# Performance work log

Hardware: AMD Instinct MI355X
Metric: run time of the kernel (lower is better)

## Reference

```python
import jax, jax.numpy as jnp
import numpy as np

N_LAB = 8   # number of distinct node labels
E_LAB = 3   # number of distinct edge labels (bond types 1..3; 0 = no edge)
N_NODES = 95
SINKHORN_ITERS = 10


def _symmetric_adj(key, n, max_lab):
    a = jax.random.randint(key, (n, n), 0, max_lab + 1).astype(jnp.int32)
    a = jnp.triu(a, 1)
    return a + a.T  # symmetric, zero diagonal


def setup_inputs() -> dict:
    key = jax.random.key(0)
    k1, k2, k3, k4, k5, k6 = jax.random.split(key, 6)
    A1 = _symmetric_adj(k1, N_NODES, E_LAB)
    A2 = _symmetric_adj(k2, N_NODES, E_LAB)
    l1 = jax.random.randint(k3, (N_NODES,), 0, N_LAB).astype(jnp.int32)
    l2 = jax.random.randint(k4, (N_NODES,), 0, N_LAB).astype(jnp.int32)
    n_pair = N_LAB * (N_LAB - 1) // 2
    e_pair = E_LAB * (E_LAB - 1) // 2
    node_weighs = (0.011 * jax.random.uniform(k5, (n_pair + 1,))).at[-1].set(0.03)
    edge_weighs = (0.011 * jax.random.uniform(k6, (e_pair + 1,))).at[-1].set(0.02)
    return {"A1": A1, "A2": A2, "l1": l1, "l2": l2,
            "node_weighs": node_weighs.astype(jnp.float32),
            "edge_weighs": edge_weighs.astype(jnp.float32)}


def _from_weighs_to_costs(node_weighs, edge_weighs):
    cn = jax.nn.relu(node_weighs)
    ce = jax.nn.relu(edge_weighs)
    iu_n = jnp.triu_indices(N_LAB, 1)
    node_costs = jnp.zeros((N_LAB, N_LAB), cn.dtype).at[iu_n].set(cn[:-1])
    node_costs = node_costs + node_costs.T
    iu_e = jnp.triu_indices(E_LAB, 1)
    edge_costs = jnp.zeros((E_LAB, E_LAB), ce.dtype).at[iu_e].set(ce[:-1])
    edge_costs = edge_costs + edge_costs.T
    return node_costs, cn[-1], edge_costs, ce[-1]


def _eps_assign2(M, n_iter):
    # Sinkhorn-style alternating row/column normalization
    for _ in range(n_iter):
        M = M / M.sum(axis=1, keepdims=True)
        M = M / M.sum(axis=0, keepdims=True)
    return M


def _ged_forward(A1, A2, l1, l2, node_weighs, edge_weighs):
    node_costs, nodeInsDel, edge_costs, edgeInsDel = _from_weighs_to_costs(node_weighs, edge_weighs)
    n = A1.shape[0]
    m = A2.shape[0]
    Np, Mp = n + 1, m + 1

    # Padded adjacency (extra epsilon row/col, label 0 = no edge)
    a1 = jnp.zeros((Np, Np), jnp.int32).at[:n, :n].set(A1)
    a2 = jnp.zeros((Mp, Mp), jnp.int32).at[:m, :m].set(A2)

    # Full edge-pair cost table over labels {0..E}: 0<->lab = ins/del, lab<->lab' = subst
    EC = jnp.zeros((E_LAB + 1, E_LAB + 1), node_costs.dtype)
    EC = EC.at[1:, 1:].set(edge_costs)
    EC = EC.at[0, 1:].set(edgeInsDel).at[1:, 0].set(edgeInsDel)
    # (original: edgeInsDel * XOR(nonzero) + sum_{k!=l} edge_costs[k,l] * 1[a1==k+1] 1[a2==l+1])

    # T[i,j,k,l] = EC[a1[i,j], a2[k,l]]; flatten as C[j*Mp+k, i*Mp+l]
    T = EC[a1[:, :, None, None], a2[None, None, :, :]]          # (Np,Np,Mp,Mp)
    Cbig = jnp.transpose(T, (1, 2, 0, 3)).reshape(Np * Mp, Np * Mp)

    # Node cost vector on the diagonal (LSAPE layout)
    NCx = jnp.zeros((N_LAB + 1, N_LAB + 1), node_costs.dtype)
    NCx = NCx.at[:N_LAB, :N_LAB].set(node_costs)
    NCx = NCx.at[N_LAB, :N_LAB].set(nodeInsDel).at[:N_LAB, N_LAB].set(nodeInsDel)
    l1e = jnp.concatenate([l1, jnp.array([N_LAB], jnp.int32)])
    l2e = jnp.concatenate([l2, jnp.array([N_LAB], jnp.int32)])
    cvec = NCx[l1e[:, None], l2e[None, :]].reshape(-1)          # (Np*Mp,)

    # D = C with diagonal zeroed (diag of C is cvec)
    idx = jnp.arange(Np * Mp)
    Dmat = Cbig.at[idx, idx].set(0.0)

    # Sinkhorn-style soft assignment on exp(-0.5*c)
    S = _eps_assign2(jnp.exp(-0.5 * cvec.reshape(Np, Mp)), SINKHORN_ITERS)
    v = S.reshape(-1)

    ged = 0.5 * (v @ (Dmat @ v)) + cvec @ v
    return ged


def reference(A1, A2, l1, l2, node_weighs, edge_weighs):
    return _ged_forward(A1, A2, l1, l2, node_weighs, edge_weighs)
```

## Files before the change

kernel.cpp:

```cpp
#include <hip/hip_runtime.h>

#define NP 96
#define NREAL 95
#define NLAB 8
#define SINK_ITERS 10

__global__ __launch_bounds__(256) void ged_fused(
    const int* __restrict__ A1, const int* __restrict__ A2,
    const int* __restrict__ l1, const int* __restrict__ l2,
    const float* __restrict__ nodeW, const float* __restrict__ edgeW,
    float* __restrict__ out)
{
    __shared__ float Wt[9][9];
    __shared__ float NC[9][9];
    __shared__ float EC[4][4];
    __shared__ int   cnt1r[9], cnt2r[9];
    __shared__ unsigned char lab1[NREAL], lab2[NREAL];
    __shared__ int   E1p[3][4][9][9], E2p[3][4][9][9];
    __shared__ float E1f[4][9][9], E2f[4][9][9];
    __shared__ float RC[18];
    __shared__ float wfin[9][9];
    __shared__ float P1[4][9][9], T2[4][9][9];
    __shared__ float Lred[4];

    const int t = threadIdx.x;
    const int lane = t & 63;
    const int wave = t >> 6;

    if (t < 9) { cnt1r[t] = 0; cnt2r[t] = 0; }
    for (int e = t; e < 3 * 324; e += 256) {
        ((int*)E1p)[e] = 0;
        ((int*)E2p)[e] = 0;
    }

    if (t < 81) {
        int r = t / 9, c = t % 9;
        float v;
        if (r == c) v = 0.f;
        else if (r == NLAB || c == NLAB) v = fmaxf(nodeW[28], 0.f);
        else {
            int rr = min(r, c), cc = max(r, c);
            int p = rr * (15 - rr) / 2 + (cc - rr - 1);
            v = fmaxf(nodeW[p], 0.f);
        }
        NC[r][c] = v;
        Wt[r][c] = expf(-0.5f * v);
    }
    if (t < 16) {
        int r = t / 4, c = t % 4;
        float v;
        if (r == c) v = 0.f;
        else if (r == 0 || c == 0) v = fmaxf(edgeW[3], 0.f);
        else {
            int rr = min(r, c) - 1, cc = max(r, c) - 1;
            int p = rr * (5 - rr) / 2 + (cc - rr - 1);
            v = fmaxf(edgeW[p], 0.f);
        }
        EC[r][c] = v;
    }
    __syncthreads();

    if (t < NREAL) {
        int a = l1[t], b = l2[t];
        lab1[t] = (unsigned char)a;
        lab2[t] = (unsigned char)b;
        atomicAdd(&cnt1r[a], 1);
        atomicAdd(&cnt2r[b], 1);
    }
    __syncthreads();

    if (wave == 0) {
        float w[9][9];
        #pragma unroll
        for (int a = 0; a < 9; ++a)
            #pragma unroll
            for (int b = 0; b < 9; ++b) w[a][b] = Wt[a][b];
        float c1[9], c2[9];
        #pragma unroll
        for (int a = 0; a < 9; ++a) {
            c1[a] = (float)cnt1r[a] + (a == 8 ? 1.f : 0.f);
            c2[a] = (float)cnt2r[a] + (a == 8 ? 1.f : 0.f);
        }
        float C[9], R[9];
        #pragma unroll
        for (int b = 0; b < 9; ++b) C[b] = 1.f;
        for (int it = 0; it < SINK_ITERS; ++it) {
            float s[9];
            #pragma unroll
            for (int b = 0; b < 9; ++b) s[b] = c2[b] * C[b];
            #pragma unroll
            for (int a = 0; a < 9; ++a) {
                float acc = 0.f;
                #pragma unroll
                for (int b = 0; b < 9; ++b) acc += w[a][b] * s[b];
                R[a] = 1.f / acc;
            }
            float r2[9];
            #pragma unroll
            for (int a = 0; a < 9; ++a) r2[a] = c1[a] * R[a];
            #pragma unroll
            for (int b = 0; b < 9; ++b) {
                float acc = 0.f;
                #pragma unroll
                for (int a = 0; a < 9; ++a) acc += w[a][b] * r2[a];
                C[b] = 1.f / acc;
            }
        }
        if (lane == 0) {
            #pragma unroll
            for (int a = 0; a < 9; ++a) { RC[a] = R[a]; RC[9 + a] = C[a]; }
        }
    } else {
        const int hw = wave - 1;
        const int lt = t - 64;
        if (lt < NREAL) {
            int p = lt;
            int alpha = lab1[p];
            const int* __restrict__ row = A1 + p * NREAL;
            for (int q = 0; q < NREAL; ++q) {
                int e = row[q];
                atomicAdd(&E1p[hw][e][alpha][lab1[q]], 1);
            }
        } else if (lt >= 96 && lt < 96 + NREAL) {
            int p = lt - 96;
            int gamma = lab2[p];
            const int* __restrict__ row = A2 + p * NREAL;
            for (int q = 0; q < NREAL; ++q) {
                int f = row[q];
                atomicAdd(&E2p[hw][f][gamma][lab2[q]], 1);
            }
        }
    }
    __syncthreads();

    for (int idx = t; idx < 324; idx += 256) {
        E1f[0][0][idx] = (float)(((int*)E1p[0])[idx] + ((int*)E1p[1])[idx] + ((int*)E1p[2])[idx]);
        E2f[0][0][idx] = (float)(((int*)E2p[0])[idx] + ((int*)E2p[1])[idx] + ((int*)E2p[2])[idx]);
    }
    __syncthreads();

    if (t < 9) {
        E1f[0][8][t] += (float)cnt1r[t];
        E1f[0][t][8] += (float)cnt1r[t];
        E2f[0][8][t] += (float)cnt2r[t];
        E2f[0][t][8] += (float)cnt2r[t];
        if (t == 8) { E1f[0][8][8] += 1.f; E2f[0][8][8] += 1.f; }
    }
    __syncthreads();

    float Lpart = 0.f;
    if (t < 81) {
        int a = t / 9, b = t % 9;
        float wv = RC[a] * Wt[a][b] * RC[9 + b];
        wfin[a][b] = wv;
        float c1f = (float)cnt1r[a] + (a == 8 ? 1.f : 0.f);
        float c2f = (float)cnt2r[b] + (b == 8 ? 1.f : 0.f);
        Lpart = c1f * c2f * NC[a][b] * wv;
    }
    #pragma unroll
    for (int off = 32; off >= 1; off >>= 1) Lpart += __shfl_xor(Lpart, off, 64);
    if (lane == 0) Lred[wave] = Lpart;
    __syncthreads();

    for (int idx = t; idx < 324; idx += 256) {
        int e = idx / 81, r = idx % 81;
        int beta = r / 9, delta = r % 9;
        float acc1 = 0.f, acc2 = 0.f;
        #pragma unroll
        for (int g = 0; g < 9; ++g) {
            acc1 += E1f[e][g][beta] * wfin[g][delta];
            acc2 += E2f[e][g][delta] * wfin[beta][g];
        }
        P1[e][beta][delta] = acc1;
        T2[e][beta][delta] = acc2;
    }
    __syncthreads();

    float qpart = 0.f;
    if (t < 16) {
        int e = t / 4, f = t % 4;
        float acc = 0.f;
        #pragma unroll
        for (int bd = 0; bd < 81; ++bd) {
            int beta = bd / 9, delta = bd % 9;
            acc += P1[e][beta][delta] * T2[f][beta][delta];
        }
        qpart = EC[e][f] * acc;
    }
    #pragma unroll
    for (int off = 8; off >= 1; off >>= 1) qpart += __shfl_xor(qpart, off, 64);
    if (t == 0) {
        float L = Lred[0] + Lred[1] + Lred[2] + Lred[3];
        out[0] = 0.5f * qpart + L;
    }
}

extern "C" void kernel_launch(void* const* d_in, const int* in_sizes, int n_in,
                              void* d_out, int out_size, void* d_ws, size_t ws_size,
                              hipStream_t stream) {
    const int*   A1    = (const int*)d_in[0];
    const int*   A2    = (const int*)d_in[1];
    const int*   l1    = (const int*)d_in[2];
    const int*   l2    = (const int*)d_in[3];
    const float* nodeW = (const float*)d_in[4];
    const float* edgeW = (const float*)d_in[5];
    float* out = (float*)d_out;

    hipLaunchKernelGGL(ged_fused, dim3(1), dim3(256), 0, stream,
                       A1, A2, l1, l2, nodeW, edgeW, out);
}
```

Measured before the change: 16.03 us.

## Double block size, split histogram rows across threads, lane-parallelize Sinkhorn

Raises the block from 256 to 512 threads, with 7 partial histogram copies instead of 3. Each adjacency row is now split between two threads, halving the serial atomic-add loop length per thread. The Sinkhorn loop on wave 0 is rewritten so each of 9 lanes owns one row and column factor and reads the others through shuffles, instead of one thread doing full 9x9 matvecs. Costs are more LDS, a longer reduction over 7 partial copies, and shuffle latency inside the Sinkhorn loop.

```diff
diff --git a/kernel.cpp b/kernel.cpp
--- a/kernel.cpp
+++ b/kernel.cpp
@@ -4,8 +4,9 @@
 #define NREAL 95
 #define NLAB 8
 #define SINK_ITERS 10
-
-__global__ __launch_bounds__(256) void ged_fused(
+#define HW 7
+
+__global__ __launch_bounds__(512) void ged_fused(
     const int* __restrict__ A1, const int* __restrict__ A2,
     const int* __restrict__ l1, const int* __restrict__ l2,
     const float* __restrict__ nodeW, const float* __restrict__ edgeW,
@@ -16,19 +17,19 @@
     __shared__ float EC[4][4];
     __shared__ int   cnt1r[9], cnt2r[9];
     __shared__ unsigned char lab1[NREAL], lab2[NREAL];
-    __shared__ int   E1p[3][4][9][9], E2p[3][4][9][9];
+    __shared__ int   E1p[HW][4][9][9], E2p[HW][4][9][9];
     __shared__ float E1f[4][9][9], E2f[4][9][9];
     __shared__ float RC[18];
     __shared__ float wfin[9][9];
     __shared__ float P1[4][9][9], T2[4][9][9];
-    __shared__ float Lred[4];
+    __shared__ float Lred[8];
 
     const int t = threadIdx.x;
     const int lane = t & 63;
     const int wave = t >> 6;
 
     if (t < 9) { cnt1r[t] = 0; cnt2r[t] = 0; }
-    for (int e = t; e < 3 * 324; e += 256) {
+    for (int e = t; e < HW * 324; e += 512) {
         ((int*)E1p)[e] = 0;
         ((int*)E2p)[e] = 0;
     }
@@ -70,72 +71,63 @@
     __syncthreads();
 
     if (wave == 0) {
-        float w[9][9];
-        #pragma unroll
-        for (int a = 0; a < 9; ++a)
+        const int a = (lane < 9) ? lane : 0;
+        float w1[9], w2[9];
+        #pragma unroll
+        for (int b = 0; b < 9; ++b) {
+            float c2b = (float)cnt2r[b] + (b == 8 ? 1.f : 0.f);
+            float c1b = (float)cnt1r[b] + (b == 8 ? 1.f : 0.f);
+            w1[b] = Wt[a][b] * c2b;
+            w2[b] = Wt[b][a] * c1b;
+        }
+        float Cm = 1.f, Rm = 1.f;
+        for (int it = 0; it < SINK_ITERS; ++it) {
+            float acc = 0.f;
             #pragma unroll
-            for (int b = 0; b < 9; ++b) w[a][b] = Wt[a][b];
-        float c1[9], c2[9];
-        #pragma unroll
-        for (int a = 0; a < 9; ++a) {
-            c1[a] = (float)cnt1r[a] + (a == 8 ? 1.f : 0.f);
-            c2[a] = (float)cnt2r[a] + (a == 8 ? 1.f : 0.f);
-        }
-        float C[9], R[9];
-        #pragma unroll
-        for (int b = 0; b < 9; ++b) C[b] = 1.f;
-        for (int it = 0; it < SINK_ITERS; ++it) {
-            float s[9];
+            for (int b = 0; b < 9; ++b) acc += w1[b] * __shfl(Cm, b, 64);
+            Rm = 1.f / acc;
+            acc = 0.f;
             #pragma unroll
-            for (int b = 0; b < 9; ++b) s[b] = c2[b] * C[b];
-            #pragma unroll
-            for (int a = 0; a < 9; ++a) {
-                float acc = 0.f;
-                #pragma unroll
-                for (int b = 0; b < 9; ++b) acc += w[a][b] * s[b];
-                R[a] = 1.f / acc;
-            }
-            float r2[9];
-            #pragma unroll
-            for (int a = 0; a < 9; ++a) r2[a] = c1[a] * R[a];
-            #pragma unroll
-            for (int b = 0; b < 9; ++b) {
-                float acc = 0.f;
-                #pragma unroll
-                for (int a = 0; a < 9; ++a) acc += w[a][b] * r2[a];
-                C[b] = 1.f / acc;
-            }
-        }
-        if (lane == 0) {
-            #pragma unroll
-            for (int a = 0; a < 9; ++a) { RC[a] = R[a]; RC[9 + a] = C[a]; }
-        }
+            for (int x = 0; x < 9; ++x) acc += w2[x] * __shfl(Rm, x, 64);
+            Cm = 1.f / acc;
+        }
+        if (lane < 9) { RC[lane] = Rm; RC[9 + lane] = Cm; }
     } else {
         const int hw = wave - 1;
         const int lt = t - 64;
-        if (lt < NREAL) {
-            int p = lt;
-            int alpha = lab1[p];
-            const int* __restrict__ row = A1 + p * NREAL;
-            for (int q = 0; q < NREAL; ++q) {
-                int e = row[q];
-                atomicAdd(&E1p[hw][e][alpha][lab1[q]], 1);
+        const unsigned char* labs = 0;
+        const int* rowp = 0;
+        int* hist = 0;
+        int p = 0, h = 0;
+        if (lt < 190) {
+            p = lt >> 1; h = lt & 1;
+            labs = lab1; rowp = A1 + p * NREAL; hist = (int*)E1p[hw];
+        } else if (lt >= 192 && lt < 382) {
+            int u = lt - 192;
+            p = u >> 1; h = u & 1;
+            labs = lab2; rowp = A2 + p * NREAL; hist = (int*)E2p[hw];
+        }
+        if (hist) {
+            const int alpha = labs[p];
+            const int base = alpha * 9;
+            const int qlo = h ? 48 : 0, qhi = h ? 95 : 48;
+            for (int q = qlo; q < qhi; ++q) {
+                int e = rowp[q];
+                atomicAdd(&hist[e * 81 + base + labs[q]], 1);
             }
-        } else if (lt >= 96 && lt < 96 + NREAL) {
-            int p = lt - 96;
-            int gamma = lab2[p];
-            const int* __restrict__ row = A2 + p * NREAL;
-            for (int q = 0; q < NREAL; ++q) {
-                int f = row[q];
-                atomicAdd(&E2p[hw][f][gamma][lab2[q]], 1);
-            }
-        }
-    }
-    __syncthreads();
-
-    for (int idx = t; idx < 324; idx += 256) {
-        E1f[0][0][idx] = (float)(((int*)E1p[0])[idx] + ((int*)E1p[1])[idx] + ((int*)E1p[2])[idx]);
-        E2f[0][0][idx] = (float)(((int*)E2p[0])[idx] + ((int*)E2p[1])[idx] + ((int*)E2p[2])[idx]);
+        }
+    }
+    __syncthreads();
+
+    for (int idx = t; idx < 324; idx += 512) {
+        int s1 = 0, s2 = 0;
+        #pragma unroll
+        for (int c = 0; c < HW; ++c) {
+            s1 += ((int*)E1p)[c * 324 + idx];
+            s2 += ((int*)E2p)[c * 324 + idx];
+        }
+        E1f[0][0][idx] = (float)s1;
+        E2f[0][0][idx] = (float)s2;
     }
     __syncthreads();
 
@@ -162,7 +154,7 @@
     if (lane == 0) Lred[wave] = Lpart;
     __syncthreads();
 
-    for (int idx = t; idx < 324; idx += 256) {
+    for (int idx = t; idx < 324; idx += 512) {
         int e = idx / 81, r = idx % 81;
         int beta = r / 9, delta = r % 9;
         float acc1 = 0.f, acc2 = 0.f;
@@ -190,7 +182,9 @@
     #pragma unroll
     for (int off = 8; off >= 1; off >>= 1) qpart += __shfl_xor(qpart, off, 64);
     if (t == 0) {
-        float L = Lred[0] + Lred[1] + Lred[2] + Lred[3];
+        float L = 0.f;
+        #pragma unroll
+        for (int w = 0; w < 8; ++w) L += Lred[w];
         out[0] = 0.5f * qpart + L;
     }
 }
@@ -206,6 +200,6 @@
     const float* edgeW = (const float*)d_in[5];
     float* out = (float*)d_out;
 
-    hipLaunchKernelGGL(ged_fused, dim3(1), dim3(256), 0, stream,
+    hipLaunchKernelGGL(ged_fused, dim3(1), dim3(512), 0, stream,
                        A1, A2, l1, l2, nodeW, edgeW, out);
 }
```

Result: slower. 17.23 us (+7.5%).
